# Optimization experiments

Measured on AMD Instinct MI355X. Metric: run time of the kernel, lower is better.

## Reference

```python
import jax, jax.numpy as jnp
import numpy as np

B, N, H, BIN, E = 16, 100, 300, 11, 20000


def setup_inputs() -> dict:
    key = jax.random.key(0)
    k1, k2, k3, k4, k5 = jax.random.split(key, 5)
    local_feats = jax.random.normal(k1, (B, N, H), dtype=jnp.float32)
    binary_feats = jax.random.normal(k2, (B, N, N, BIN), dtype=jnp.float32)
    sparse_idx = jax.random.randint(k3, (E, 3), 0, B).astype(jnp.int64)
    W1 = jax.random.normal(k4, (H + BIN, H), dtype=jnp.float32) * 0.02
    b1 = jnp.zeros((H,), dtype=jnp.float32)
    W2 = jax.random.normal(k5, (H, 1), dtype=jnp.float32) * 0.02
    b2 = jnp.zeros((1,), dtype=jnp.float32)
    return {"local_feats": local_feats, "binary_feats": binary_feats,
            "sparse_idx": sparse_idx, "W1": W1, "b1": b1, "W2": W2, "b2": b2}


def reference(local_feats, binary_feats, sparse_idx, W1, b1, W2, b2):
    # local_pair[b,i,j] = local_feats[b,j] + local_feats[b,i]  -> [B,N,N,H]
    local_pair = local_feats[:, None, :, :] + local_feats[:, :, None, :]
    all_feats = jnp.concatenate([local_pair, binary_feats], axis=-1)  # [B,N,N,H+BIN]
    att = jax.nn.relu(jnp.einsum('bijk,kh->bijh', all_feats, W1) + b1)  # [B,N,N,H]
    score = jax.nn.sigmoid(jnp.einsum('bijh,ho->bijo', att, W2) + b2)   # [B,N,N,1]
    # weighted sum over dim j (torch dim=2 of [B,1,N,H]*[B,N,N,1])
    global_feats = jnp.sum(local_feats[:, None, :, :] * score, axis=2)  # [B,N,H]
    bb, ii, jj = sparse_idx[:, 0], sparse_idx[:, 1], sparse_idx[:, 2]
    global_pair = global_feats[bb, ii] + global_feats[bb, jj]  # [E,H]
    local_pair_g = local_pair[bb, ii, jj]                      # [E,H]
    return (local_pair_g, global_pair)
```

## Files before the change

### kernel.cpp

```cpp
#include <hip/hip_runtime.h>

#define BB 16
#define NN 100
#define HH 300
#define EE 20000

typedef __bf16 bf16x8 __attribute__((ext_vector_type(8)));
typedef float f32x4 __attribute__((ext_vector_type(4)));

__device__ __forceinline__ unsigned short f2bf_u(float v) {
  const unsigned u = __builtin_bit_cast(unsigned, v);
  return (unsigned short)((u + 0x7FFFu + ((u >> 16) & 1u)) >> 16);
}
__device__ __forceinline__ __bf16 f2bf(float v) {
  unsigned short s = f2bf_u(v);
  return __builtin_bit_cast(__bf16, s);
}

#define OFF_U 0
#define OFF_GF 1920000
#define OFF_XB 2227200
#define OFF_W1T 3251200
#define OFF_W1BT 3445760

__global__ __launch_bounds__(256) void k_prep(const float* __restrict__ X,
                                              const float* __restrict__ W1,
                                              const int* __restrict__ sp,
                                              float* __restrict__ out,
                                              unsigned short* __restrict__ Xb,
                                              unsigned short* __restrict__ W1T,
                                              unsigned short* __restrict__ W1BT) {
  const int gtid = (int)blockIdx.x * 256 + (int)threadIdx.x;
  const int gs = (int)gridDim.x * 256;

  for (int e = gtid; e < 1600 * 320; e += gs) {
    const int r = e / 320, k = e - r * 320;
    Xb[e] = f2bf_u((k < 300) ? X[r * 300 + k] : 0.f);
  }
  for (int e = gtid; e < 304 * 320; e += gs) {
    const int j = e / 320, k = e - j * 320;
    W1T[e] = f2bf_u((k < 300 && j < 300) ? W1[k * 300 + j] : 0.f);
  }
  for (int e = gtid; e < 19 * 512; e += gs) {
    const int nt = e / 512;
    const int r = (e & 511) >> 5;
    const int k = e & 31;
    const int h = nt * 16 + r;
    float v = 0.f;
    if (k < 11 && h < 300) v = W1[(300 + k) * 300 + h];
    W1BT[e] = f2bf_u(v);
  }
  {
    const float4* __restrict__ X4 = (const float4*)X;
    float4* __restrict__ out0 = (float4*)out;
    for (int idx = gtid; idx < EE * 75; idx += gs) {
      const int e = idx / 75;
      const int c = idx - e * 75;
      const int b = sp[e * 3 + 0];
      const int ii = sp[e * 3 + 1];
      const int jj = sp[e * 3 + 2];
      const float4 xi = X4[(b * 100 + ii) * 75 + c];
      const float4 xj = X4[(b * 100 + jj) * 75 + c];
      out0[idx] =
          make_float4(xi.x + xj.x, xi.y + xj.y, xi.z + xj.z, xi.w + xj.w);
    }
  }
}

__global__ __launch_bounds__(256) void k_proj_mfma(
    const unsigned short* __restrict__ Xb,
    const unsigned short* __restrict__ W1T, const float* __restrict__ b1,
    float* __restrict__ U) {
  const int wave = threadIdx.x >> 6;
  const int lane = threadIdx.x & 63;
  const int tile = blockIdx.x * 4 + wave;
  const int mt = tile / 19;
  const int nt = tile - mt * 19;
  const int r0 = mt * 16;
  const int n0 = nt * 16;
  const int l15 = lane & 15;
  const int lk = (lane >> 4) * 8;

  f32x4 acc = {0.f, 0.f, 0.f, 0.f};
  const unsigned short* ap = Xb + (r0 + l15) * 320 + lk;
  const unsigned short* bp = W1T + (n0 + l15) * 320 + lk;
#pragma unroll
  for (int kc = 0; kc < 10; ++kc) {
    const bf16x8 av = *reinterpret_cast<const bf16x8*>(ap + kc * 32);
    const bf16x8 bv = *reinterpret_cast<const bf16x8*>(bp + kc * 32);
    acc = __builtin_amdgcn_mfma_f32_16x16x32_bf16(av, bv, acc, 0, 0, 0);
  }
  const int h = n0 + l15;
  if (h < 300) {
    const float hb = 0.5f * b1[h];
    const int rbase = r0 + (lane >> 4) * 4;
#pragma unroll
    for (int reg = 0; reg < 4; ++reg)
      U[(rbase + reg) * 300 + h] = acc[reg] + hb;
  }
}

__global__ __launch_bounds__(448) void k_scoreGF(
    const float* __restrict__ X, const float* __restrict__ U,
    const float* __restrict__ W2, const float* __restrict__ b2,
    const float* __restrict__ Bin, const unsigned short* __restrict__ W1BT,
    float* __restrict__ gf) {
  __shared__ float s_bin[1100];
  __shared__ float s_score[100];

  const int bi = (int)blockIdx.x;
  const int b = bi >> 4;
  const int i = bi & 15;
  const int tid = (int)threadIdx.x;

  for (int t = tid; t < 1100; t += 448)
    s_bin[t] = Bin[(size_t)(b * 100 + i) * 1100 + t];
  __syncthreads();

  const int jt = tid >> 6;
  const int lane = tid & 63;
  const int l15 = lane & 15;
  const int lk = (lane >> 4) * 8;

  float ui[19], w2[19];
#pragma unroll
  for (int nt = 0; nt < 19; ++nt) {
    const int h = nt * 16 + l15;
    const int hc = (h < 300) ? h : 299;
    ui[nt] = U[(b * 100 + i) * 300 + hc];
    w2[nt] = (h < 300) ? W2[h] : 0.f;
  }

  bf16x8 af;
  const int jrow_l = jt * 16 + l15;
#pragma unroll
  for (int t = 0; t < 8; ++t) {
    const int k = lk + t;
    af[t] = (jrow_l < 100 && k < 11) ? f2bf(s_bin[jrow_l * 11 + k])
                                     : f2bf(0.f);
  }

  const int jbase = jt * 16 + (lane >> 4) * 4;
  int jrow[4];
#pragma unroll
  for (int reg = 0; reg < 4; ++reg)
    jrow[reg] = (jbase + reg < 100) ? (jbase + reg) : 99;

  float jacc[4] = {0.f, 0.f, 0.f, 0.f};
  for (int nt = 0; nt < 19; ++nt) {
    const bf16x8 bf =
        *reinterpret_cast<const bf16x8*>(W1BT + (nt * 16 + l15) * 32 + lk);
    const int h = nt * 16 + l15;
    const int hc = (h < 300) ? h : 299;
    f32x4 cin;
#pragma unroll
    for (int reg = 0; reg < 4; ++reg)
      cin[reg] = ui[nt] + U[(b * 100 + jrow[reg]) * 300 + hc];
    f32x4 d = __builtin_amdgcn_mfma_f32_16x16x32_bf16(af, bf, cin, 0, 0, 0);
#pragma unroll
    for (int reg = 0; reg < 4; ++reg)
      jacc[reg] = fmaf(fmaxf(d[reg], 0.f), w2[nt], jacc[reg]);
  }

  const float b2v = b2[0];
#pragma unroll
  for (int reg = 0; reg < 4; ++reg) {
    float p = jacc[reg];
#pragma unroll
    for (int m = 8; m >= 1; m >>= 1) p += __shfl_xor(p, m, 64);
    if (l15 == 0) {
      const int j = jbase + reg;
      if (j < 100) s_score[j] = 1.f / (1.f + __expf(-(p + b2v)));
    }
  }
  __syncthreads();

  if (tid < 300) {
    const float* __restrict__ Xr = X + b * 100 * 300 + tid;
    float g0 = 0.f, g1 = 0.f, g2 = 0.f, g3 = 0.f, g4 = 0.f;
#pragma unroll
    for (int jl = 0; jl < 100; jl += 5) {
      g0 = fmaf(Xr[(jl + 0) * 300], s_score[jl + 0], g0);
      g1 = fmaf(Xr[(jl + 1) * 300], s_score[jl + 1], g1);
      g2 = fmaf(Xr[(jl + 2) * 300], s_score[jl + 2], g2);
      g3 = fmaf(Xr[(jl + 3) * 300], s_score[jl + 3], g3);
      g4 = fmaf(Xr[(jl + 4) * 300], s_score[jl + 4], g4);
    }
    gf[bi * 300 + tid] = ((g0 + g1) + (g2 + g3)) + g4;
  }
}

__global__ __launch_bounds__(256) void k_out1(const int* __restrict__ sp,
                                              const float* __restrict__ gf,
                                              float* __restrict__ out) {
  const float4* __restrict__ G4 = (const float4*)gf;
  float4* __restrict__ out1 = (float4*)out + EE * 75;

  for (int idx = (int)blockIdx.x * 256 + (int)threadIdx.x; idx < EE * 75;
       idx += (int)gridDim.x * 256) {
    const int e = idx / 75;
    const int c = idx - e * 75;
    const int b = sp[e * 3 + 0];
    const int ii = sp[e * 3 + 1];
    const int jj = sp[e * 3 + 2];
    const float4 g1 = G4[(b * 16 + ii) * 75 + c];
    const float4 g2 = G4[(b * 16 + jj) * 75 + c];
    out1[idx] =
        make_float4(g1.x + g2.x, g1.y + g2.y, g1.z + g2.z, g1.w + g2.w);
  }
}

extern "C" void kernel_launch(void* const* d_in, const int* in_sizes, int n_in,
                              void* d_out, int out_size, void* d_ws,
                              size_t ws_size, hipStream_t stream) {
  const float* X   = (const float*)d_in[0];
  const float* Bin = (const float*)d_in[1];
  const int*   sp  = (const int*)d_in[2];
  const float* W1  = (const float*)d_in[3];
  const float* b1  = (const float*)d_in[4];
  const float* W2  = (const float*)d_in[5];
  const float* b2  = (const float*)d_in[6];
  float* out = (float*)d_out;

  char* wsb = (char*)d_ws;
  float* U = (float*)(wsb + OFF_U);
  float* gf = (float*)(wsb + OFF_GF);
  unsigned short* Xb = (unsigned short*)(wsb + OFF_XB);
  unsigned short* W1T = (unsigned short*)(wsb + OFF_W1T);
  unsigned short* W1BT = (unsigned short*)(wsb + OFF_W1BT);

  k_prep<<<2048, 256, 0, stream>>>(X, W1, sp, out, Xb, W1T, W1BT);
  k_proj_mfma<<<475, 256, 0, stream>>>(Xb, W1T, b1, U);
  k_scoreGF<<<256, 448, 0, stream>>>(X, U, W2, b2, Bin, W1BT, gf);
  k_out1<<<2048, 256, 0, stream>>>(sp, gf, out);
}
```

Before: 42.17 us.

## Fuse projection GEMM into score kernel and merge output gathers

Removes the separate X→bf16 conversion and the U projection kernel. Each score block now recomputes the needed rows of X·W1 on the fly with MFMA, converting X to bf16 in registers, and computes the i-row projection into shared memory. The local-pair gather moves from the prep kernel into the final output kernel, leaving three launches instead of four. The cost is redundant GEMM work: each block recomputes the projection for all 100 j rows, roughly 16x duplication across the i-blocks.

```diff
diff --git a/kernel.cpp b/kernel.cpp
--- a/kernel.cpp
+++ b/kernel.cpp
@@ -17,26 +17,15 @@
   return __builtin_bit_cast(__bf16, s);
 }
 
-#define OFF_U 0
-#define OFF_GF 1920000
-#define OFF_XB 2227200
-#define OFF_W1T 3251200
-#define OFF_W1BT 3445760
-
-__global__ __launch_bounds__(256) void k_prep(const float* __restrict__ X,
-                                              const float* __restrict__ W1,
-                                              const int* __restrict__ sp,
-                                              float* __restrict__ out,
-                                              unsigned short* __restrict__ Xb,
-                                              unsigned short* __restrict__ W1T,
-                                              unsigned short* __restrict__ W1BT) {
+#define OFF_GF 0
+#define OFF_W1T 307200
+#define OFF_W1BT 501760
+
+__global__ __launch_bounds__(256) void k_prepW(const float* __restrict__ W1,
+                                               unsigned short* __restrict__ W1T,
+                                               unsigned short* __restrict__ W1BT) {
   const int gtid = (int)blockIdx.x * 256 + (int)threadIdx.x;
   const int gs = (int)gridDim.x * 256;
-
-  for (int e = gtid; e < 1600 * 320; e += gs) {
-    const int r = e / 320, k = e - r * 320;
-    Xb[e] = f2bf_u((k < 300) ? X[r * 300 + k] : 0.f);
-  }
   for (int e = gtid; e < 304 * 320; e += gs) {
     const int j = e / 320, k = e - j * 320;
     W1T[e] = f2bf_u((k < 300 && j < 300) ? W1[k * 300 + j] : 0.f);
@@ -50,119 +39,116 @@
     if (k < 11 && h < 300) v = W1[(300 + k) * 300 + h];
     W1BT[e] = f2bf_u(v);
   }
-  {
-    const float4* __restrict__ X4 = (const float4*)X;
-    float4* __restrict__ out0 = (float4*)out;
-    for (int idx = gtid; idx < EE * 75; idx += gs) {
-      const int e = idx / 75;
-      const int c = idx - e * 75;
-      const int b = sp[e * 3 + 0];
-      const int ii = sp[e * 3 + 1];
-      const int jj = sp[e * 3 + 2];
-      const float4 xi = X4[(b * 100 + ii) * 75 + c];
-      const float4 xj = X4[(b * 100 + jj) * 75 + c];
-      out0[idx] =
-          make_float4(xi.x + xj.x, xi.y + xj.y, xi.z + xj.z, xi.w + xj.w);
-    }
-  }
-}
-
-__global__ __launch_bounds__(256) void k_proj_mfma(
-    const unsigned short* __restrict__ Xb,
-    const unsigned short* __restrict__ W1T, const float* __restrict__ b1,
-    float* __restrict__ U) {
-  const int wave = threadIdx.x >> 6;
-  const int lane = threadIdx.x & 63;
-  const int tile = blockIdx.x * 4 + wave;
-  const int mt = tile / 19;
-  const int nt = tile - mt * 19;
-  const int r0 = mt * 16;
-  const int n0 = nt * 16;
-  const int l15 = lane & 15;
-  const int lk = (lane >> 4) * 8;
-
-  f32x4 acc = {0.f, 0.f, 0.f, 0.f};
-  const unsigned short* ap = Xb + (r0 + l15) * 320 + lk;
-  const unsigned short* bp = W1T + (n0 + l15) * 320 + lk;
-#pragma unroll
-  for (int kc = 0; kc < 10; ++kc) {
-    const bf16x8 av = *reinterpret_cast<const bf16x8*>(ap + kc * 32);
-    const bf16x8 bv = *reinterpret_cast<const bf16x8*>(bp + kc * 32);
-    acc = __builtin_amdgcn_mfma_f32_16x16x32_bf16(av, bv, acc, 0, 0, 0);
-  }
-  const int h = n0 + l15;
-  if (h < 300) {
-    const float hb = 0.5f * b1[h];
-    const int rbase = r0 + (lane >> 4) * 4;
-#pragma unroll
-    for (int reg = 0; reg < 4; ++reg)
-      U[(rbase + reg) * 300 + h] = acc[reg] + hb;
-  }
-}
-
-__global__ __launch_bounds__(448) void k_scoreGF(
-    const float* __restrict__ X, const float* __restrict__ U,
-    const float* __restrict__ W2, const float* __restrict__ b2,
-    const float* __restrict__ Bin, const unsigned short* __restrict__ W1BT,
-    float* __restrict__ gf) {
+}
+
+__global__ __launch_bounds__(448) void k_score2(
+    const float* __restrict__ X, const float* __restrict__ Bin,
+    const float* __restrict__ b1, const float* __restrict__ W2,
+    const float* __restrict__ b2, const unsigned short* __restrict__ W1T,
+    const unsigned short* __restrict__ W1BT, float* __restrict__ gf) {
   __shared__ float s_bin[1100];
+  __shared__ float s_ui[304];
   __shared__ float s_score[100];
 
   const int bi = (int)blockIdx.x;
   const int b = bi >> 4;
   const int i = bi & 15;
   const int tid = (int)threadIdx.x;
-
-  for (int t = tid; t < 1100; t += 448)
-    s_bin[t] = Bin[(size_t)(b * 100 + i) * 1100 + t];
-  __syncthreads();
-
-  const int jt = tid >> 6;
+  const int wv = tid >> 6;
   const int lane = tid & 63;
   const int l15 = lane & 15;
   const int lk = (lane >> 4) * 8;
 
-  float ui[19], w2[19];
+  for (int t = tid; t < 1100; t += 448)
+    s_bin[t] = Bin[(size_t)(b * 100 + i) * 1100 + t];
+
+  bf16x8 xf[10];
+  auto loadA = [&](int jt) {
+    int row = jt * 16 + l15;
+    if (row > 99) row = 99;
+    const float* __restrict__ xr = X + (size_t)(b * 100 + row) * 300 + lk;
+#pragma unroll
+    for (int kc = 0; kc < 10; ++kc) {
+      if (lk + kc * 32 + 7 < 300) {
+        const float4 a = *reinterpret_cast<const float4*>(xr + kc * 32);
+        const float4 c = *reinterpret_cast<const float4*>(xr + kc * 32 + 4);
+        xf[kc][0] = f2bf(a.x); xf[kc][1] = f2bf(a.y);
+        xf[kc][2] = f2bf(a.z); xf[kc][3] = f2bf(a.w);
+        xf[kc][4] = f2bf(c.x); xf[kc][5] = f2bf(c.y);
+        xf[kc][6] = f2bf(c.z); xf[kc][7] = f2bf(c.w);
+      } else {
+#pragma unroll
+        for (int t = 0; t < 8; ++t) {
+          const int k = lk + kc * 32 + t;
+          xf[kc][t] = f2bf((k < 300) ? xr[kc * 32 + t] : 0.f);
+        }
+      }
+    }
+  };
+
+  loadA(0);
+  const int ir = i & 3;
+#pragma unroll
+  for (int r = 0; r < 3; ++r) {
+    const int nt = wv + 7 * r;
+    if (nt < 19) {
+      f32x4 ut = {0.f, 0.f, 0.f, 0.f};
+      const unsigned short* wp = W1T + (nt * 16 + l15) * 320 + lk;
+#pragma unroll
+      for (int kc = 0; kc < 10; ++kc) {
+        const bf16x8 wt = *reinterpret_cast<const bf16x8*>(wp + kc * 32);
+        ut = __builtin_amdgcn_mfma_f32_16x16x32_bf16(xf[kc], wt, ut, 0, 0, 0);
+      }
+      const float uv = (ir == 0) ? ut[0] : (ir == 1) ? ut[1]
+                        : (ir == 2) ? ut[2] : ut[3];
+      const float uival = __shfl(uv, ((i >> 2) << 4) + l15, 64);
+      if (lane < 16) {
+        const int h = nt * 16 + lane;
+        s_ui[h] = uival + ((h < 300) ? b1[h] : 0.f);
+      }
+    }
+  }
+  __syncthreads();
+
+  loadA(wv);
+  bf16x8 af;
+  const int jrl = wv * 16 + l15;
+#pragma unroll
+  for (int t = 0; t < 8; ++t) {
+    const int k = lk + t;
+    af[t] = (jrl < 100 && k < 11) ? f2bf(s_bin[jrl * 11 + k]) : f2bf(0.f);
+  }
+  float w2r[19];
 #pragma unroll
   for (int nt = 0; nt < 19; ++nt) {
     const int h = nt * 16 + l15;
-    const int hc = (h < 300) ? h : 299;
-    ui[nt] = U[(b * 100 + i) * 300 + hc];
-    w2[nt] = (h < 300) ? W2[h] : 0.f;
-  }
-
-  bf16x8 af;
-  const int jrow_l = jt * 16 + l15;
-#pragma unroll
-  for (int t = 0; t < 8; ++t) {
-    const int k = lk + t;
-    af[t] = (jrow_l < 100 && k < 11) ? f2bf(s_bin[jrow_l * 11 + k])
-                                     : f2bf(0.f);
-  }
-
-  const int jbase = jt * 16 + (lane >> 4) * 4;
-  int jrow[4];
-#pragma unroll
-  for (int reg = 0; reg < 4; ++reg)
-    jrow[reg] = (jbase + reg < 100) ? (jbase + reg) : 99;
+    w2r[nt] = (h < 300) ? W2[h] : 0.f;
+  }
 
   float jacc[4] = {0.f, 0.f, 0.f, 0.f};
+#pragma unroll 2
   for (int nt = 0; nt < 19; ++nt) {
-    const bf16x8 bf =
+    f32x4 ut = {0.f, 0.f, 0.f, 0.f};
+    const unsigned short* wp = W1T + (nt * 16 + l15) * 320 + lk;
+#pragma unroll
+    for (int kc = 0; kc < 10; ++kc) {
+      const bf16x8 wt = *reinterpret_cast<const bf16x8*>(wp + kc * 32);
+      ut = __builtin_amdgcn_mfma_f32_16x16x32_bf16(xf[kc], wt, ut, 0, 0, 0);
+    }
+    const float uih = s_ui[nt * 16 + l15];
+    f32x4 cin;
+#pragma unroll
+    for (int reg = 0; reg < 4; ++reg) cin[reg] = ut[reg] + uih;
+    const bf16x8 wb =
         *reinterpret_cast<const bf16x8*>(W1BT + (nt * 16 + l15) * 32 + lk);
-    const int h = nt * 16 + l15;
-    const int hc = (h < 300) ? h : 299;
-    f32x4 cin;
+    const f32x4 d = __builtin_amdgcn_mfma_f32_16x16x32_bf16(af, wb, cin, 0, 0, 0);
 #pragma unroll
     for (int reg = 0; reg < 4; ++reg)
-      cin[reg] = ui[nt] + U[(b * 100 + jrow[reg]) * 300 + hc];
-    f32x4 d = __builtin_amdgcn_mfma_f32_16x16x32_bf16(af, bf, cin, 0, 0, 0);
-#pragma unroll
-    for (int reg = 0; reg < 4; ++reg)
-      jacc[reg] = fmaf(fmaxf(d[reg], 0.f), w2[nt], jacc[reg]);
+      jacc[reg] = fmaf(fmaxf(d[reg], 0.f), w2r[nt], jacc[reg]);
   }
 
   const float b2v = b2[0];
+  const int jbase = wv * 16 + (lane >> 4) * 4;
 #pragma unroll
   for (int reg = 0; reg < 4; ++reg) {
     float p = jacc[reg];
@@ -176,7 +162,7 @@
   __syncthreads();
 
   if (tid < 300) {
-    const float* __restrict__ Xr = X + b * 100 * 300 + tid;
+    const float* __restrict__ Xr = X + (size_t)b * 100 * 300 + tid;
     float g0 = 0.f, g1 = 0.f, g2 = 0.f, g3 = 0.f, g4 = 0.f;
 #pragma unroll
     for (int jl = 0; jl < 100; jl += 5) {
@@ -190,11 +176,14 @@
   }
 }
 
-__global__ __launch_bounds__(256) void k_out1(const int* __restrict__ sp,
-                                              const float* __restrict__ gf,
-                                              float* __restrict__ out) {
+__global__ __launch_bounds__(256) void k_out(const float* __restrict__ X,
+                                             const int* __restrict__ sp,
+                                             const float* __restrict__ gf,
+                                             float* __restrict__ out) {
+  const float4* __restrict__ X4 = (const float4*)X;
   const float4* __restrict__ G4 = (const float4*)gf;
-  float4* __restrict__ out1 = (float4*)out + EE * 75;
+  float4* __restrict__ out0 = (float4*)out;
+  float4* __restrict__ out1 = out0 + EE * 75;
 
   for (int idx = (int)blockIdx.x * 256 + (int)threadIdx.x; idx < EE * 75;
        idx += (int)gridDim.x * 256) {
@@ -203,6 +192,11 @@
     const int b = sp[e * 3 + 0];
     const int ii = sp[e * 3 + 1];
     const int jj = sp[e * 3 + 2];
+
+    const float4 xi = X4[(b * 100 + ii) * 75 + c];
+    const float4 xj = X4[(b * 100 + jj) * 75 + c];
+    out0[idx] = make_float4(xi.x + xj.x, xi.y + xj.y, xi.z + xj.z, xi.w + xj.w);
+
     const float4 g1 = G4[(b * 16 + ii) * 75 + c];
     const float4 g2 = G4[(b * 16 + jj) * 75 + c];
     out1[idx] =
@@ -223,14 +217,11 @@
   float* out = (float*)d_out;
 
   char* wsb = (char*)d_ws;
-  float* U = (float*)(wsb + OFF_U);
   float* gf = (float*)(wsb + OFF_GF);
-  unsigned short* Xb = (unsigned short*)(wsb + OFF_XB);
   unsigned short* W1T = (unsigned short*)(wsb + OFF_W1T);
   unsigned short* W1BT = (unsigned short*)(wsb + OFF_W1BT);
 
-  k_prep<<<2048, 256, 0, stream>>>(X, W1, sp, out, Xb, W1T, W1BT);
-  k_proj_mfma<<<475, 256, 0, stream>>>(Xb, W1T, b1, U);
-  k_scoreGF<<<256, 448, 0, stream>>>(X, U, W2, b2, Bin, W1BT, gf);
-  k_out1<<<2048, 256, 0, stream>>>(sp, gf, out);
-}
+  k_prepW<<<128, 256, 0, stream>>>(W1, W1T, W1BT);
+  k_score2<<<256, 448, 0, stream>>>(X, Bin, b1, W2, b2, W1T, W1BT, gf);
+  k_out<<<2048, 256, 0, stream>>>(X, sp, gf, out);
+}
```

After: 75.13 us. +78.2%, slower.

## Split score/global-feature kernel across j-quarters and hidden halves, reduce partials in gather

Applied to the files above, without the earlier changes.

The score+global-feature kernel now launches four blocks per (b,i) row, each covering 32 of the j columns. Within a block, two waves split the 19 hidden tiles and their partial dot products are combined through shared memory before the sigmoid. Each block writes a partial global-feature vector for its j-quarter, and the gather kernel sums the four partials for both indices. This raises parallelism from 256 large blocks to 1024 smaller ones, at the cost of four times more global-feature reads in the final gather and extra shared-memory syncs.

```diff
diff --git a/kernel.cpp b/kernel.cpp
--- a/kernel.cpp
+++ b/kernel.cpp
@@ -17,11 +17,11 @@
   return __builtin_bit_cast(__bf16, s);
 }
 
-#define OFF_U 0
-#define OFF_GF 1920000
-#define OFF_XB 2227200
-#define OFF_W1T 3251200
-#define OFF_W1BT 3445760
+#define OFF_GFQ 0
+#define OFF_W1T 1228800
+#define OFF_W1BT 1423360
+#define OFF_XB 1442816
+#define OFF_U 2466816
 
 __global__ __launch_bounds__(256) void k_prep(const float* __restrict__ X,
                                               const float* __restrict__ W1,
@@ -100,100 +100,109 @@
   }
 }
 
-__global__ __launch_bounds__(448) void k_scoreGF(
+__global__ __launch_bounds__(256) void k_scoreQ(
     const float* __restrict__ X, const float* __restrict__ U,
     const float* __restrict__ W2, const float* __restrict__ b2,
     const float* __restrict__ Bin, const unsigned short* __restrict__ W1BT,
-    float* __restrict__ gf) {
-  __shared__ float s_bin[1100];
-  __shared__ float s_score[100];
-
-  const int bi = (int)blockIdx.x;
+    float* __restrict__ gfQ) {
+  __shared__ float s_bin[32 * 11];
+  __shared__ float s_part[2][2][16];
+  __shared__ float s_score[32];
+
+  const int q = (int)blockIdx.x & 3;
+  const int bi = (int)blockIdx.x >> 2;
   const int b = bi >> 4;
   const int i = bi & 15;
+  const int j0 = q * 32;
   const int tid = (int)threadIdx.x;
-
-  for (int t = tid; t < 1100; t += 448)
-    s_bin[t] = Bin[(size_t)(b * 100 + i) * 1100 + t];
-  __syncthreads();
-
-  const int jt = tid >> 6;
+  const int wv = tid >> 6;
+  const int jt_l = wv >> 1;
+  const int nth = wv & 1;
   const int lane = tid & 63;
   const int l15 = lane & 15;
   const int lk = (lane >> 4) * 8;
 
-  float ui[19], w2[19];
-#pragma unroll
-  for (int nt = 0; nt < 19; ++nt) {
-    const int h = nt * 16 + l15;
-    const int hc = (h < 300) ? h : 299;
-    ui[nt] = U[(b * 100 + i) * 300 + hc];
-    w2[nt] = (h < 300) ? W2[h] : 0.f;
-  }
+  for (int t = tid; t < 352; t += 256) {
+    const int jl = t / 11, k = t - jl * 11;
+    const int j = (j0 + jl < 100) ? (j0 + jl) : 99;
+    s_bin[t] = Bin[((size_t)(b * 100 + i) * 100 + j) * 11 + k];
+  }
+  __syncthreads();
 
   bf16x8 af;
-  const int jrow_l = jt * 16 + l15;
 #pragma unroll
   for (int t = 0; t < 8; ++t) {
     const int k = lk + t;
-    af[t] = (jrow_l < 100 && k < 11) ? f2bf(s_bin[jrow_l * 11 + k])
-                                     : f2bf(0.f);
-  }
-
-  const int jbase = jt * 16 + (lane >> 4) * 4;
+    af[t] = (k < 11) ? f2bf(s_bin[(jt_l * 16 + l15) * 11 + k]) : f2bf(0.f);
+  }
+
+  const int jbase = j0 + jt_l * 16 + (lane >> 4) * 4;
   int jrow[4];
 #pragma unroll
   for (int reg = 0; reg < 4; ++reg)
     jrow[reg] = (jbase + reg < 100) ? (jbase + reg) : 99;
 
+  const float* __restrict__ Ui = U + (b * 100 + i) * 300;
   float jacc[4] = {0.f, 0.f, 0.f, 0.f};
-  for (int nt = 0; nt < 19; ++nt) {
+
+  auto step = [&](int nt) {
     const bf16x8 bf =
         *reinterpret_cast<const bf16x8*>(W1BT + (nt * 16 + l15) * 32 + lk);
     const int h = nt * 16 + l15;
     const int hc = (h < 300) ? h : 299;
+    const float ui = Ui[hc];
+    const float w2v = (h < 300) ? W2[h] : 0.f;
     f32x4 cin;
 #pragma unroll
     for (int reg = 0; reg < 4; ++reg)
-      cin[reg] = ui[nt] + U[(b * 100 + jrow[reg]) * 300 + hc];
-    f32x4 d = __builtin_amdgcn_mfma_f32_16x16x32_bf16(af, bf, cin, 0, 0, 0);
+      cin[reg] = ui + U[(b * 100 + jrow[reg]) * 300 + hc];
+    const f32x4 d = __builtin_amdgcn_mfma_f32_16x16x32_bf16(af, bf, cin, 0, 0, 0);
 #pragma unroll
     for (int reg = 0; reg < 4; ++reg)
-      jacc[reg] = fmaf(fmaxf(d[reg], 0.f), w2[nt], jacc[reg]);
-  }
-
-  const float b2v = b2[0];
+      jacc[reg] = fmaf(fmaxf(d[reg], 0.f), w2v, jacc[reg]);
+  };
+  if (nth == 0) {
+#pragma unroll
+    for (int t = 0; t < 10; ++t) step(t);
+  } else {
+#pragma unroll
+    for (int t = 0; t < 9; ++t) step(10 + t);
+  }
+
 #pragma unroll
   for (int reg = 0; reg < 4; ++reg) {
     float p = jacc[reg];
 #pragma unroll
     for (int m = 8; m >= 1; m >>= 1) p += __shfl_xor(p, m, 64);
-    if (l15 == 0) {
-      const int j = jbase + reg;
-      if (j < 100) s_score[j] = 1.f / (1.f + __expf(-(p + b2v)));
-    }
+    if (l15 == 0) s_part[jt_l][nth][(lane >> 4) * 4 + reg] = p;
   }
   __syncthreads();
 
-  if (tid < 300) {
-    const float* __restrict__ Xr = X + b * 100 * 300 + tid;
-    float g0 = 0.f, g1 = 0.f, g2 = 0.f, g3 = 0.f, g4 = 0.f;
-#pragma unroll
-    for (int jl = 0; jl < 100; jl += 5) {
+  if (tid < 32) {
+    const int jt = tid >> 4, jx = tid & 15;
+    const float p = s_part[jt][0][jx] + s_part[jt][1][jx] + b2[0];
+    s_score[tid] = 1.f / (1.f + __expf(-p));
+  }
+  __syncthreads();
+
+  const int jmax = (q == 3) ? 4 : 32;
+  for (int col = tid; col < 300; col += 256) {
+    const float* __restrict__ Xr = X + (size_t)(b * 100 + j0) * 300 + col;
+    float g0 = 0.f, g1 = 0.f, g2 = 0.f, g3 = 0.f;
+    for (int jl = 0; jl < jmax; jl += 4) {
       g0 = fmaf(Xr[(jl + 0) * 300], s_score[jl + 0], g0);
       g1 = fmaf(Xr[(jl + 1) * 300], s_score[jl + 1], g1);
       g2 = fmaf(Xr[(jl + 2) * 300], s_score[jl + 2], g2);
       g3 = fmaf(Xr[(jl + 3) * 300], s_score[jl + 3], g3);
-      g4 = fmaf(Xr[(jl + 4) * 300], s_score[jl + 4], g4);
     }
-    gf[bi * 300 + tid] = ((g0 + g1) + (g2 + g3)) + g4;
+    gfQ[((size_t)bi * 4 + q) * 300 + col] = (g0 + g1) + (g2 + g3);
   }
 }
 
 __global__ __launch_bounds__(256) void k_out1(const int* __restrict__ sp,
-                                              const float* __restrict__ gf,
+                                              const float* __restrict__ gfQ,
                                               float* __restrict__ out) {
-  const float4* __restrict__ G4 = (const float4*)gf;
+  const float4* __restrict__ G4 = (const float4*)gfQ;
   float4* __restrict__ out1 = (float4*)out + EE * 75;
 
   for (int idx = (int)blockIdx.x * 256 + (int)threadIdx.x; idx < EE * 75;
@@ -203,10 +212,20 @@
     const int b = sp[e * 3 + 0];
     const int ii = sp[e * 3 + 1];
     const int jj = sp[e * 3 + 2];
-    const float4 g1 = G4[(b * 16 + ii) * 75 + c];
-    const float4 g2 = G4[(b * 16 + jj) * 75 + c];
-    out1[idx] =
-        make_float4(g1.x + g2.x, g1.y + g2.y, g1.z + g2.z, g1.w + g2.w);
+
+    const int gi = (b * 16 + ii) * 300 + c;
+    const int gj = (b * 16 + jj) * 300 + c;
+    float4 a = make_float4(0.f, 0.f, 0.f, 0.f);
+#pragma unroll
+    for (int t = 0; t < 4; ++t) {
+      const float4 g1 = G4[gi + t * 75];
+      const float4 g2 = G4[gj + t * 75];
+      a.x += g1.x + g2.x;
+      a.y += g1.y + g2.y;
+      a.z += g1.z + g2.z;
+      a.w += g1.w + g2.w;
+    }
+    out1[idx] = a;
   }
 }
 
@@ -223,14 +242,14 @@
   float* out = (float*)d_out;
 
   char* wsb = (char*)d_ws;
-  float* U = (float*)(wsb + OFF_U);
-  float* gf = (float*)(wsb + OFF_GF);
-  unsigned short* Xb = (unsigned short*)(wsb + OFF_XB);
+  float* gfQ = (float*)(wsb + OFF_GFQ);
   unsigned short* W1T = (unsigned short*)(wsb + OFF_W1T);
   unsigned short* W1BT = (unsigned short*)(wsb + OFF_W1BT);
+  unsigned short* Xb = (unsigned short*)(wsb + OFF_XB);
+  float* U = (float*)(wsb + OFF_U);
 
   k_prep<<<2048, 256, 0, stream>>>(X, W1, sp, out, Xb, W1T, W1BT);
   k_proj_mfma<<<475, 256, 0, stream>>>(Xb, W1T, b1, U);
-  k_scoreGF<<<256, 448, 0, stream>>>(X, U, W2, b2, Bin, W1BT, gf);
-  k_out1<<<2048, 256, 0, stream>>>(sp, gf, out);
-}
+  k_scoreQ<<<1024, 256, 0, stream>>>(X, U, W2, b2, Bin, W1BT, gfQ);
+  k_out1<<<2048, 256, 0, stream>>>(sp, gfQ, out);
+}
```

Result: slower. 48.15 us (+14.2%).

## Split score kernel across 16 waves over hidden tiles and j-quarters

Applied to the files above, without the earlier changes.

The score/global-feature kernel now launches 1024 threads per block instead of 448. Each j-tile's 19 hidden tiles are split across two waves, and partial sums are combined through shared memory. The weighted sum over j is also split into four quarters, each reduced through shared memory, so more threads work per block. Workspace offsets are reordered. This targets latency in a kernel with only 256 blocks, at the cost of extra barriers and shared-memory reductions.

```diff
diff --git a/kernel.cpp b/kernel.cpp
--- a/kernel.cpp
+++ b/kernel.cpp
@@ -17,11 +17,11 @@
   return __builtin_bit_cast(__bf16, s);
 }
 
-#define OFF_U 0
-#define OFF_GF 1920000
-#define OFF_XB 2227200
-#define OFF_W1T 3251200
-#define OFF_W1BT 3445760
+#define OFF_GF 0
+#define OFF_W1T 307200
+#define OFF_W1BT 501760
+#define OFF_XB 521216
+#define OFF_U 1545216
 
 __global__ __launch_bounds__(256) void k_prep(const float* __restrict__ X,
                                               const float* __restrict__ W1,
@@ -100,93 +100,112 @@
   }
 }
 
-__global__ __launch_bounds__(448) void k_scoreGF(
+__global__ __launch_bounds__(1024) void k_scoreGF2(
     const float* __restrict__ X, const float* __restrict__ U,
     const float* __restrict__ W2, const float* __restrict__ b2,
     const float* __restrict__ Bin, const unsigned short* __restrict__ W1BT,
     float* __restrict__ gf) {
   __shared__ float s_bin[1100];
+  __shared__ float s_part[7][2][16];
   __shared__ float s_score[100];
+  __shared__ float s_gpart[4][300];
 
   const int bi = (int)blockIdx.x;
   const int b = bi >> 4;
   const int i = bi & 15;
   const int tid = (int)threadIdx.x;
-
-  for (int t = tid; t < 1100; t += 448)
-    s_bin[t] = Bin[(size_t)(b * 100 + i) * 1100 + t];
-  __syncthreads();
-
-  const int jt = tid >> 6;
+  const int wv = tid >> 6;
+  const int jt = wv >> 1;
+  const int nth = wv & 1;
   const int lane = tid & 63;
   const int l15 = lane & 15;
   const int lk = (lane >> 4) * 8;
 
-  float ui[19], w2[19];
-#pragma unroll
-  for (int nt = 0; nt < 19; ++nt) {
-    const int h = nt * 16 + l15;
-    const int hc = (h < 300) ? h : 299;
-    ui[nt] = U[(b * 100 + i) * 300 + hc];
-    w2[nt] = (h < 300) ? W2[h] : 0.f;
-  }
-
-  bf16x8 af;
-  const int jrow_l = jt * 16 + l15;
-#pragma unroll
-  for (int t = 0; t < 8; ++t) {
-    const int k = lk + t;
-    af[t] = (jrow_l < 100 && k < 11) ? f2bf(s_bin[jrow_l * 11 + k])
-                                     : f2bf(0.f);
-  }
-
-  const int jbase = jt * 16 + (lane >> 4) * 4;
-  int jrow[4];
-#pragma unroll
-  for (int reg = 0; reg < 4; ++reg)
-    jrow[reg] = (jbase + reg < 100) ? (jbase + reg) : 99;
-
-  float jacc[4] = {0.f, 0.f, 0.f, 0.f};
-  for (int nt = 0; nt < 19; ++nt) {
-    const bf16x8 bf =
-        *reinterpret_cast<const bf16x8*>(W1BT + (nt * 16 + l15) * 32 + lk);
-    const int h = nt * 16 + l15;
-    const int hc = (h < 300) ? h : 299;
-    f32x4 cin;
+  for (int t = tid; t < 1100; t += 1024)
+    s_bin[t] = Bin[(size_t)(b * 100 + i) * 1100 + t];
+  __syncthreads();
+
+  if (jt < 7) {
+    bf16x8 af;
+    const int jrl = jt * 16 + l15;
+    const int jr_cl = (jrl < 100) ? jrl : 99;
+#pragma unroll
+    for (int t = 0; t < 8; ++t) {
+      const int k = lk + t;
+      af[t] = (k < 11) ? f2bf(s_bin[jr_cl * 11 + k]) : f2bf(0.f);
+    }
+
+    const int jbase = jt * 16 + (lane >> 4) * 4;
+    int jrow[4];
 #pragma unroll
     for (int reg = 0; reg < 4; ++reg)
-      cin[reg] = ui[nt] + U[(b * 100 + jrow[reg]) * 300 + hc];
-    f32x4 d = __builtin_amdgcn_mfma_f32_16x16x32_bf16(af, bf, cin, 0, 0, 0);
-#pragma unroll
-    for (int reg = 0; reg < 4; ++reg)
-      jacc[reg] = fmaf(fmaxf(d[reg], 0.f), w2[nt], jacc[reg]);
-  }
-
-  const float b2v = b2[0];
-#pragma unroll
-  for (int reg = 0; reg < 4; ++reg) {
-    float p = jacc[reg];
-#pragma unroll
-    for (int m = 8; m >= 1; m >>= 1) p += __shfl_xor(p, m, 64);
-    if (l15 == 0) {
-      const int j = jbase + reg;
-      if (j < 100) s_score[j] = 1.f / (1.f + __expf(-(p + b2v)));
-    }
-  }
-  __syncthreads();
-
-  if (tid < 300) {
-    const float* __restrict__ Xr = X + b * 100 * 300 + tid;
+      jrow[reg] = (jbase + reg < 100) ? (jbase + reg) : 99;
+
+    const float* __restrict__ Ui = U + (b * 100 + i) * 300;
+    float jacc[4] = {0.f, 0.f, 0.f, 0.f};
+
+    auto step = [&](int nt) {
+      const bf16x8 bf =
+          *reinterpret_cast<const bf16x8*>(W1BT + (nt * 16 + l15) * 32 + lk);
+      const int h = nt * 16 + l15;
+      const int hc = (h < 300) ? h : 299;
+      const float ui = Ui[hc];
+      const float w2v = (h < 300) ? W2[h] : 0.f;
+      f32x4 cin;
+#pragma unroll
+      for (int reg = 0; reg < 4; ++reg)
+        cin[reg] = ui + U[(b * 100 + jrow[reg]) * 300 + hc];
+      const f32x4 d =
+          __builtin_amdgcn_mfma_f32_16x16x32_bf16(af, bf, cin, 0, 0, 0);
+#pragma unroll
+      for (int reg = 0; reg < 4; ++reg)
+        jacc[reg] = fmaf(fmaxf(d[reg], 0.f), w2v, jacc[reg]);
+    };
+    if (nth == 0) {
+#pragma unroll
+      for (int t = 0; t < 10; ++t) step(t);
+    } else {
+#pragma unroll
+      for (int t = 0; t < 9; ++t) step(10 + t);
+    }
+
+#pragma unroll
+    for (int reg = 0; reg < 4; ++reg) {
+      float p = jacc[reg];
+#pragma unroll
+      for (int m = 8; m >= 1; m >>= 1) p += __shfl_xor(p, m, 64);
+      if (l15 == 0) s_part[jt][nth][(lane >> 4) * 4 + reg] = p;
+    }
+  }
+  __syncthreads();
+
+  if (tid < 100) {
+    const float p = s_part[tid >> 4][0][tid & 15] +
+                    s_part[tid >> 4][1][tid & 15] + b2[0];
+    s_score[tid] = 1.f / (1.f + __expf(-p));
+  }
+  __syncthreads();
+
+  for (int item = tid; item < 1200; item += 1024) {
+    const int jq = item / 300;
+    const int col = item - jq * 300;
+    const float* __restrict__ Xr = X + (size_t)(b * 100 + jq * 25) * 300 + col;
     float g0 = 0.f, g1 = 0.f, g2 = 0.f, g3 = 0.f, g4 = 0.f;
 #pragma unroll
-    for (int jl = 0; jl < 100; jl += 5) {
-      g0 = fmaf(Xr[(jl + 0) * 300], s_score[jl + 0], g0);
-      g1 = fmaf(Xr[(jl + 1) * 300], s_score[jl + 1], g1);
-      g2 = fmaf(Xr[(jl + 2) * 300], s_score[jl + 2], g2);
-      g3 = fmaf(Xr[(jl + 3) * 300], s_score[jl + 3], g3);
-      g4 = fmaf(Xr[(jl + 4) * 300], s_score[jl + 4], g4);
-    }
-    gf[bi * 300 + tid] = ((g0 + g1) + (g2 + g3)) + g4;
+    for (int jl = 0; jl < 25; jl += 5) {
+      g0 = fmaf(Xr[(jl + 0) * 300], s_score[jq * 25 + jl + 0], g0);
+      g1 = fmaf(Xr[(jl + 1) * 300], s_score[jq * 25 + jl + 1], g1);
+      g2 = fmaf(Xr[(jl + 2) * 300], s_score[jq * 25 + jl + 2], g2);
+      g3 = fmaf(Xr[(jl + 3) * 300], s_score[jq * 25 + jl + 3], g3);
+      g4 = fmaf(Xr[(jl + 4) * 300], s_score[jq * 25 + jl + 4], g4);
+    }
+    s_gpart[jq][col] = ((g0 + g1) + (g2 + g3)) + g4;
+  }
+  __syncthreads();
+
+  for (int col = tid; col < 300; col += 1024) {
+    gf[bi * 300 + col] = (s_gpart[0][col] + s_gpart[1][col]) +
+                         (s_gpart[2][col] + s_gpart[3][col]);
   }
 }
 
@@ -223,14 +242,14 @@
   float* out = (float*)d_out;
 
   char* wsb = (char*)d_ws;
-  float* U = (float*)(wsb + OFF_U);
   float* gf = (float*)(wsb + OFF_GF);
-  unsigned short* Xb = (unsigned short*)(wsb + OFF_XB);
   unsigned short* W1T = (unsigned short*)(wsb + OFF_W1T);
   unsigned short* W1BT = (unsigned short*)(wsb + OFF_W1BT);
+  unsigned short* Xb = (unsigned short*)(wsb + OFF_XB);
+  float* U = (float*)(wsb + OFF_U);
 
   k_prep<<<2048, 256, 0, stream>>>(X, W1, sp, out, Xb, W1T, W1BT);
   k_proj_mfma<<<475, 256, 0, stream>>>(Xb, W1T, b1, U);
-  k_scoreGF<<<256, 448, 0, stream>>>(X, U, W2, b2, Bin, W1BT, gf);
+  k_scoreGF2<<<256, 1024, 0, stream>>>(X, U, W2, b2, Bin, W1BT, gf);
   k_out1<<<2048, 256, 0, stream>>>(sp, gf, out);
 }
```

Result: faster. 37.86 us (-10.2%).
